# Kernel tuning notes

Measured on AMD Instinct MI355X. Metric: run time of the kernel, lower is better.

The kernel has to match this reference:

```python
import jax, jax.numpy as jnp
import numpy as np

B, S, F_, D, H, L, OUT = 2, 1024, 240, 512, 6, 6, 512
NH = 16
DH = D // NH
EPS = 1e-6  # fast_transformers causal-linear eps
LN_EPS = 1e-5  # torch LayerNorm default


def layernorm(x, g, b):
    m = x.mean(-1, keepdims=True)
    v = ((x - m) ** 2).mean(-1, keepdims=True)
    return (x - m) * jax.lax.rsqrt(v + LN_EPS) * g + b


def causal_linear_attn(q, k, v):
    # q,k,v: [B,S,NH,DH]; feature map phi(x)=elu(x)+1 (fast_transformers default)
    Q = jax.nn.elu(q) + 1.0
    K = jax.nn.elu(k) + 1.0
    # running sum of outer products K_i V_i^T -> [B,S,NH,DH,DH]
    kv = jnp.cumsum(jnp.einsum('bshd,bshm->bshdm', K, v), axis=1)
    num = jnp.einsum('bshd,bshdm->bshm', Q, kv)
    Z = 1.0 / (jnp.einsum('bshd,bshd->bsh', Q, jnp.cumsum(K, axis=1)) + EPS)
    return num * Z[..., None]


def setup_inputs() -> dict:
    key = jax.random.key(0)
    ks = iter(jax.random.split(key, 16))

    def w(shape, s=0.02):
        return (s * jax.random.normal(next(ks), shape)).astype(jnp.float32)

    f32 = jnp.float32
    return {
        'x': jax.random.normal(next(ks), (B, S, F_), dtype=f32),
        'g_in': jnp.ones((F_,), f32), 'b_in': jnp.zeros((F_,), f32),
        'W_pre': w((F_, D)), 'b_pre': jnp.zeros((D,), f32),
        'Wq': w((L, D, D)), 'bq': jnp.zeros((L, D), f32),
        'Wk': w((L, D, D)), 'bk': jnp.zeros((L, D), f32),
        'Wv': w((L, D, D)), 'bv': jnp.zeros((L, D), f32),
        'Wo': w((L, D, D)), 'bo': jnp.zeros((L, D), f32),
        'W1': w((L, D, D)), 'bf1': jnp.zeros((L, D), f32),  # feed_forward_dimensions == hidden_sz
        'W2': w((L, D, D)), 'bf2': jnp.zeros((L, D), f32),
        'ln1_g': jnp.ones((L, D), f32), 'ln1_b': jnp.zeros((L, D), f32),
        'ln2_g': jnp.ones((L, D), f32), 'ln2_b': jnp.zeros((L, D), f32),
        'lnf_g': jnp.ones((D,), f32), 'lnf_b': jnp.zeros((D,), f32),
        'W_post': w((D, OUT)), 'b_post': jnp.zeros((OUT,), f32),
    }


def reference(x, g_in, b_in, W_pre, b_pre, Wq, bq, Wk, bk, Wv, bv, Wo, bo,
              W1, bf1, W2, bf2, ln1_g, ln1_b, ln2_g, ln2_b, lnf_g, lnf_b,
              W_post, b_post):
    # input norm + pre projection
    h = layernorm(x, g_in, b_in) @ W_pre + b_pre  # [B,S,D]
    # fast_transformers post-norm encoder layers
    for l in range(L):
        q = (h @ Wq[l] + bq[l]).reshape(B, S, NH, DH)
        k = (h @ Wk[l] + bk[l]).reshape(B, S, NH, DH)
        v = (h @ Wv[l] + bv[l]).reshape(B, S, NH, DH)
        a = causal_linear_attn(q, k, v).reshape(B, S, D) @ Wo[l] + bo[l]
        h = layernorm(h + a, ln1_g[l], ln1_b[l])
        y = jax.nn.relu(h @ W1[l] + bf1[l]) @ W2[l] + bf2[l]
        h = layernorm(h + y, ln2_g[l], ln2_b[l])
    # final encoder norm, then post projection
    h = layernorm(h, lnf_g, lnf_b)
    return h @ W_post + b_post
```

## Files before the change

### kernel.cpp

```cpp
#include <hip/hip_runtime.h>
#include <hip/hip_bf16.h>
#include <cmath>

#define NROW 2048
#define DMODEL 512
#define FIN 240
#define FINPAD 256
#define NHEAD 16
#define DHEAD 32
#define CHUNK 64
#define NCHUNK 16
#define NLAYER 6
#define SEQ 1024
#define QKVLD 1536

typedef __attribute__((ext_vector_type(8))) short bf16x8;
typedef __attribute__((ext_vector_type(4))) float f32x4;

#define MFMA_BF16 __builtin_amdgcn_mfma_f32_16x16x32_bf16

__device__ __forceinline__ float phi(float x) {
    return x > 0.f ? x + 1.f : expf(x);
}

__device__ __forceinline__ void load_lds16(const void* g, void* l) {
    __builtin_amdgcn_global_load_lds(
        (const __attribute__((address_space(1))) void*)g,
        (__attribute__((address_space(3))) void*)l, 16, 0, 0);
}

__global__ __launch_bounds__(256) void ln_kernel(
    const float* __restrict__ in, const float* __restrict__ res,
    const float* __restrict__ g, const float* __restrict__ b,
    float* __restrict__ out, __hip_bfloat16* __restrict__ outb,
    int C, int Cpad) {
    int row = blockIdx.x;
    int tid = threadIdx.x;
    const float* xr = in + (size_t)row * C;
    const float* rr = res ? res + (size_t)row * C : nullptr;
    float vals[2];
    float sum = 0.f, sq = 0.f;
#pragma unroll
    for (int i = 0; i < 2; ++i) {
        int c = tid + i * 256;
        float v = 0.f;
        if (c < C) { v = xr[c]; if (rr) v += rr[c]; }
        vals[i] = v;
        sum += v; sq += v * v;
    }
#pragma unroll
    for (int off = 32; off > 0; off >>= 1) {
        sum += __shfl_xor(sum, off, 64);
        sq  += __shfl_xor(sq,  off, 64);
    }
    __shared__ float red[8];
    int wv = tid >> 6, ln = tid & 63;
    if (ln == 0) { red[wv] = sum; red[4 + wv] = sq; }
    __syncthreads();
    sum = red[0] + red[1] + red[2] + red[3];
    sq  = red[4] + red[5] + red[6] + red[7];
    float mean = sum / (float)C;
    float var  = sq / (float)C - mean * mean;
    float rstd = rsqrtf(var + 1e-5f);
#pragma unroll
    for (int i = 0; i < 2; ++i) {
        int c = tid + i * 256;
        float y = (vals[i] - mean) * rstd;
        if (c < C) {
            y = y * g[c] + b[c];
            if (out) out[(size_t)row * C + c] = y;
        }
        if (outb && c < Cpad)
            outb[(size_t)row * Cpad + c] = __float2bfloat16(c < C ? y : 0.f);
    }
}

template<int RELU, int WF32, int WBF16, int PHI, int K>
__global__ __launch_bounds__(256) void gemm_bf16_kernel(
    const __hip_bfloat16* __restrict__ A, const __hip_bfloat16* __restrict__ Bt,
    const float* __restrict__ bias,
    float* __restrict__ C, __hip_bfloat16* __restrict__ Cb,
    int N) {
    constexpr int NSTEP = K / 64;
    __shared__ __align__(16) __hip_bfloat16 As[4][32][64];
    __shared__ __align__(16) __hip_bfloat16 Bs[4][64][64];
    const int tid = threadIdx.x, lane = tid & 63, w = tid >> 6;
    const int nN = N >> 6;
    const int bm = (blockIdx.x / nN) * 32;
    const int bn = (blockIdx.x % nN) * 64;

    const int srow  = lane >> 3;
    const int sslot = (lane & 7) ^ srow;
    const size_t aoff = (size_t)srow * K + (size_t)sslot * 8;
    const __hip_bfloat16* gA  = A  + (size_t)(bm + w * 8) * K + aoff;
    const __hip_bfloat16* gB0 = Bt + (size_t)(bn + w * 8) * K + aoff;
    const __hip_bfloat16* gB1 = Bt + (size_t)(bn + 32 + w * 8) * K + aoff;

#define STAGE(t) do { \
        load_lds16(gA  + (size_t)(t) * 64, &As[(t) & 3][w * 8][0]); \
        load_lds16(gB0 + (size_t)(t) * 64, &Bs[(t) & 3][w * 8][0]); \
        load_lds16(gB1 + (size_t)(t) * 64, &Bs[(t) & 3][32 + w * 8][0]); \
    } while (0)

    const int wm = (w >> 1) << 4, wn = (w & 1) << 5;
    const int fr = lane & 15, fq = lane >> 4;
    const int sw = fr & 7;
    const int e0 = ((fq      ^ sw) << 3);
    const int e1 = (((fq | 4) ^ sw) << 3);
    f32x4 acc0 = {0.f, 0.f, 0.f, 0.f}, acc1 = acc0;

    STAGE(0); STAGE(1); STAGE(2);
#pragma unroll
    for (int t = 0; t < NSTEP; ++t) {
        if (NSTEP - t >= 3)      asm volatile("s_waitcnt vmcnt(6)" ::: "memory");
        else if (NSTEP - t == 2) asm volatile("s_waitcnt vmcnt(3)" ::: "memory");
        else                     asm volatile("s_waitcnt vmcnt(0)" ::: "memory");
        __builtin_amdgcn_s_barrier();
        __builtin_amdgcn_sched_barrier(0);
        if (t + 3 < NSTEP) STAGE(t + 3);
        const int b = t & 3;
        bf16x8 a0  = *(const bf16x8*)&As[b][wm + fr][e0];
        bf16x8 a1  = *(const bf16x8*)&As[b][wm + fr][e1];
        bf16x8 b00 = *(const bf16x8*)&Bs[b][wn + fr][e0];
        bf16x8 b01 = *(const bf16x8*)&Bs[b][wn + fr][e1];
        bf16x8 b10 = *(const bf16x8*)&Bs[b][wn + 16 + fr][e0];
        bf16x8 b11 = *(const bf16x8*)&Bs[b][wn + 16 + fr][e1];
        acc0 = MFMA_BF16(a0, b00, acc0, 0, 0, 0);
        acc1 = MFMA_BF16(a0, b10, acc1, 0, 0, 0);
        acc0 = MFMA_BF16(a1, b01, acc0, 0, 0, 0);
        acc1 = MFMA_BF16(a1, b11, acc1, 0, 0, 0);
    }
#undef STAGE

    const int orow = bm + wm + (fq << 2);
    const int ocol = bn + wn + fr;
    float bv0 = bias[ocol], bv1 = bias[ocol + 16];
#pragma unroll
    for (int r = 0; r < 4; ++r) {
        float v0 = acc0[r] + bv0;
        float v1 = acc1[r] + bv1;
        if (RELU) { v0 = fmaxf(v0, 0.f); v1 = fmaxf(v1, 0.f); }
        if (PHI) {
            if (ocol < 1024)      v0 = phi(v0);
            if (ocol + 16 < 1024) v1 = phi(v1);
        }
        if (WF32) {
            C[(size_t)(orow + r) * N + ocol]      = v0;
            C[(size_t)(orow + r) * N + ocol + 16] = v1;
        }
        if (WBF16) {
            Cb[(size_t)(orow + r) * N + ocol]      = __float2bfloat16(v0);
            Cb[(size_t)(orow + r) * N + ocol + 16] = __float2bfloat16(v1);
        }
    }
}

__global__ __launch_bounds__(256) void wconv_kernel(
    const float* __restrict__ W_pre, const float* __restrict__ Wq,
    const float* __restrict__ Wk, const float* __restrict__ Wv,
    const float* __restrict__ Wo, const float* __restrict__ W1,
    const float* __restrict__ W2, const float* __restrict__ W_post,
    const float* __restrict__ bq, const float* __restrict__ bk,
    const float* __restrict__ bv, float* __restrict__ qkvbias,
    __hip_bfloat16* wpre_t, __hip_bfloat16* wqkv_t, __hip_bfloat16* wo_t,
    __hip_bfloat16* w1_t, __hip_bfloat16* w2_t, __hip_bfloat16* wpost_t) {
    __shared__ float tile[64][65];
    int tb = blockIdx.x;
    if (tb >= 2400) {
        int l = tb - 2400;
        for (int i = threadIdx.x; i < 512; i += 256) {
            qkvbias[l * QKVLD + i]        = bq[l * DMODEL + i];
            qkvbias[l * QKVLD + 512 + i]  = bk[l * DMODEL + i];
            qkvbias[l * QKVLD + 1024 + i] = bv[l * DMODEL + i];
        }
        return;
    }
    const float* src; __hip_bfloat16* dst; int K, Kpad, kt, nt;
    if (tb < 32) {
        src = W_pre; dst = wpre_t; K = FIN; Kpad = FINPAD;
        kt = tb >> 3; nt = tb & 7;
    } else {
        int t2 = tb - 32; int mat = t2 >> 6; int tt = t2 & 63;
        kt = tt >> 3; nt = tt & 7; K = 512; Kpad = 512;
        if (mat == 36) { src = W_post; dst = wpost_t; }
        else {
            int l = mat / 6, j = mat % 6;
            const size_t WSZ = 262144;
            switch (j) {
                case 0: src = Wq + l * WSZ; dst = wqkv_t + l * 786432;          break;
                case 1: src = Wk + l * WSZ; dst = wqkv_t + l * 786432 + 262144; break;
                case 2: src = Wv + l * WSZ; dst = wqkv_t + l * 786432 + 524288; break;
                case 3: src = Wo + l * WSZ; dst = wo_t + l * WSZ;               break;
                case 4: src = W1 + l * WSZ; dst = w1_t + l * WSZ;               break;
                default: src = W2 + l * WSZ; dst = w2_t + l * WSZ;              break;
            }
        }
    }
    const int N = 512;
    int t = threadIdx.x;
    int k0 = kt * 64, n0 = nt * 64;
#pragma unroll
    for (int i = 0; i < 16; ++i) {
        int kk = (t >> 6) * 16 + i;
        int nn = t & 63;
        int k = k0 + kk;
        tile[kk][nn] = (k < K) ? src[(size_t)k * N + n0 + nn] : 0.f;
    }
    __syncthreads();
#pragma unroll
    for (int i = 0; i < 16; ++i) {
        int nn = (t >> 6) * 16 + i;
        int kk = t & 63;
        dst[(size_t)(n0 + nn) * Kpad + k0 + kk] = __float2bfloat16(tile[kk][nn]);
    }
}

__global__ __launch_bounds__(64) void attn_state_kernel(
    const __hip_bfloat16* __restrict__ qkvb,
    float* __restrict__ Sg, float* __restrict__ ksumg) {
    __shared__ __hip_bfloat16 Kt[32][72];
    __shared__ __hip_bfloat16 Vt[32][72];
    int c = blockIdx.x, hh = blockIdx.y, b = blockIdx.z;
    int t = threadIdx.x;
    int sub = t >> 2, slot = t & 3;
    size_t rb = ((size_t)(b * SEQ + c * CHUNK)) * QKVLD + hh * DHEAD;
#pragma unroll
    for (int it = 0; it < 4; ++it) {
        int s = it * 16 + sub;
        bf16x8 kv = *(const bf16x8*)&qkvb[rb + (size_t)s * QKVLD + 512 + slot * 8];
        bf16x8 vv = *(const bf16x8*)&qkvb[rb + (size_t)s * QKVLD + 1024 + slot * 8];
#pragma unroll
        for (int i = 0; i < 8; ++i) {
            Kt[slot * 8 + i][s] = ((const __hip_bfloat16*)&kv)[i];
            Vt[slot * 8 + i][s] = ((const __hip_bfloat16*)&vv)[i];
        }
    }
    __syncthreads();
    int fr = t & 15, fq = t >> 4;
    f32x4 a00 = {0.f,0.f,0.f,0.f}, a01 = a00, a10 = a00, a11 = a00;
#pragma unroll
    for (int ks = 0; ks < 2; ++ks) {
        bf16x8 v0 = *(const bf16x8*)&Vt[fr][ks * 32 + fq * 8];
        bf16x8 v1 = *(const bf16x8*)&Vt[16 + fr][ks * 32 + fq * 8];
        bf16x8 k0 = *(const bf16x8*)&Kt[fr][ks * 32 + fq * 8];
        bf16x8 k1 = *(const bf16x8*)&Kt[16 + fr][ks * 32 + fq * 8];
        a00 = MFMA_BF16(v0, k0, a00, 0, 0, 0);
        a01 = MFMA_BF16(v0, k1, a01, 0, 0, 0);
        a10 = MFMA_BF16(v1, k0, a10, 0, 0, 0);
        a11 = MFMA_BF16(v1, k1, a11, 0, 0, 0);
    }
    size_t ob = ((size_t)((b * NHEAD + hh) * NCHUNK + c)) * 1024;
#pragma unroll
    for (int r = 0; r < 4; ++r) {
        int m0 = fq * 4 + r;
        Sg[ob + (size_t)m0 * 32 + fr]             = a00[r];
        Sg[ob + (size_t)m0 * 32 + 16 + fr]        = a01[r];
        Sg[ob + (size_t)(16 + m0) * 32 + fr]      = a10[r];
        Sg[ob + (size_t)(16 + m0) * 32 + 16 + fr] = a11[r];
    }
    if (t < 32) {
        float s_ = 0.f;
        for (int s = 0; s < CHUNK; ++s) s_ += __bfloat162float(Kt[t][s]);
        ksumg[((size_t)((b * NHEAD + hh) * NCHUNK + c)) * 32 + t] = s_;
    }
}

__global__ __launch_bounds__(256) void attn_out_kernel(
    const __hip_bfloat16* __restrict__ qkvb,
    const float* __restrict__ Sg, const float* __restrict__ ksumg,
    __hip_bfloat16* __restrict__ out) {
    __shared__ __hip_bfloat16 Qs[64][40];
    __shared__ __hip_bfloat16 Ks[64][40];
    __shared__ __hip_bfloat16 Vt[32][72];
    __shared__ __hip_bfloat16 Awb[64][72];
    __shared__ __hip_bfloat16 Stb[32][40];
    __shared__ float den[64];
    __shared__ float ksml[32];
    int c = blockIdx.x, hh = blockIdx.y, b = blockIdx.z;
    int tid = threadIdx.x, lane = tid & 63, w = tid >> 6;
    size_t rb = ((size_t)(b * SEQ + c * CHUNK)) * QKVLD + hh * DHEAD;
    {
        int row = tid >> 2, slot = tid & 3;
        *(bf16x8*)&Qs[row][slot * 8] =
            *(const bf16x8*)&qkvb[rb + (size_t)row * QKVLD + slot * 8];
        *(bf16x8*)&Ks[row][slot * 8] =
            *(const bf16x8*)&qkvb[rb + (size_t)row * QKVLD + 512 + slot * 8];
        bf16x8 vv = *(const bf16x8*)&qkvb[rb + (size_t)row * QKVLD + 1024 + slot * 8];
        if (row < 64) {
#pragma unroll
            for (int i = 0; i < 8; ++i)
                Vt[slot * 8 + i][row] = ((const __hip_bfloat16*)&vv)[i];
        }
    }
    size_t sb = ((size_t)((b * NHEAD + hh) * NCHUNK)) * 1024;
    {
        f32x4 st = {0.f, 0.f, 0.f, 0.f};
        for (int cp = 0; cp < c; ++cp)
            st += *(const f32x4*)&Sg[sb + (size_t)cp * 1024 + tid * 4];
        int m = tid >> 3, d0 = (tid & 7) * 4;
#pragma unroll
        for (int i = 0; i < 4; ++i) Stb[m][d0 + i] = __float2bfloat16(st[i]);
    }
    if (tid < 32) {
        size_t kb = ((size_t)((b * NHEAD + hh) * NCHUNK)) * 32;
        float s_ = 0.f;
        for (int cp = 0; cp < c; ++cp) s_ += ksumg[kb + cp * 32 + tid];
        ksml[tid] = s_;
    }
    __syncthreads();
    int fr = lane & 15, fq = lane >> 4;
    bf16x8 aQ = *(const bf16x8*)&Qs[w * 16 + fr][fq * 8];
    f32x4 p[4];
#pragma unroll
    for (int j = 0; j < 4; ++j) {
        f32x4 z = {0.f, 0.f, 0.f, 0.f};
        bf16x8 bK = *(const bf16x8*)&Ks[j * 16 + fr][fq * 8];
        p[j] = MFMA_BF16(aQ, bK, z, 0, 0, 0);
    }
    float rs[4] = {0.f, 0.f, 0.f, 0.f};
#pragma unroll
    for (int j = 0; j < 4; ++j) {
        int tcol = j * 16 + fr;
#pragma unroll
        for (int r = 0; r < 4; ++r) {
            int s = w * 16 + fq * 4 + r;
            float val = (tcol <= s) ? p[j][r] : 0.f;
            p[j][r] = val;
            rs[r] += val;
        }
    }
#pragma unroll
    for (int off = 8; off > 0; off >>= 1) {
#pragma unroll
        for (int r = 0; r < 4; ++r) rs[r] += __shfl_xor(rs[r], off, 64);
    }
    if (fr == 0) {
#pragma unroll
        for (int r = 0; r < 4; ++r) den[w * 16 + fq * 4 + r] = rs[r];
    }
#pragma unroll
    for (int j = 0; j < 4; ++j)
#pragma unroll
        for (int r = 0; r < 4; ++r)
            Awb[w * 16 + fq * 4 + r][j * 16 + fr] = __float2bfloat16(p[j][r]);
    __syncthreads();
    if (tid < 64) {
        float dq = den[tid];
        float dst_ = 0.f;
#pragma unroll
        for (int d = 0; d < 32; ++d)
            dst_ += __bfloat162float(Qs[tid][d]) * ksml[d];
        den[tid] = 1.f / (dq + dst_ + 1e-6f);
    }
    __syncthreads();
    size_t orb = ((size_t)(b * SEQ + c * CHUNK)) * DMODEL + hh * DHEAD;
#pragma unroll
    for (int mf = 0; mf < 2; ++mf) {
        f32x4 acc = {0.f, 0.f, 0.f, 0.f};
        bf16x8 bS = *(const bf16x8*)&Stb[mf * 16 + fr][fq * 8];
        acc = MFMA_BF16(aQ, bS, acc, 0, 0, 0);
#pragma unroll
        for (int ks = 0; ks < 2; ++ks) {
            bf16x8 aA = *(const bf16x8*)&Awb[w * 16 + fr][ks * 32 + fq * 8];
            bf16x8 bV = *(const bf16x8*)&Vt[mf * 16 + fr][ks * 32 + fq * 8];
            acc = MFMA_BF16(aA, bV, acc, 0, 0, 0);
        }
#pragma unroll
        for (int r = 0; r < 4; ++r) {
            int s = w * 16 + fq * 4 + r;
            out[orb + (size_t)s * DMODEL + mf * 16 + fr] =
                __float2bfloat16(acc[r] * den[s]);
        }
    }
}

template<int R, int WF, int WB, int PHI, int K>
static inline void gemm(const __hip_bfloat16* A, const __hip_bfloat16* Bt,
                        const float* bias, float* C, __hip_bfloat16* Cb,
                        int M, int N, hipStream_t s) {
    gemm_bf16_kernel<R, WF, WB, PHI, K><<<(M / 32) * (N / 64), 256, 0, s>>>(A, Bt, bias, C, Cb, N);
}

extern "C" void kernel_launch(void* const* d_in, const int* in_sizes, int n_in,
                              void* d_out, int out_size, void* d_ws, size_t ws_size,
                              hipStream_t stream) {
    const float* x      = (const float*)d_in[0];
    const float* g_in   = (const float*)d_in[1];
    const float* b_in   = (const float*)d_in[2];
    const float* W_pre  = (const float*)d_in[3];
    const float* b_pre  = (const float*)d_in[4];
    const float* Wq     = (const float*)d_in[5];
    const float* bq     = (const float*)d_in[6];
    const float* Wk     = (const float*)d_in[7];
    const float* bk     = (const float*)d_in[8];
    const float* Wv     = (const float*)d_in[9];
    const float* bv     = (const float*)d_in[10];
    const float* Wo     = (const float*)d_in[11];
    const float* bo     = (const float*)d_in[12];
    const float* W1     = (const float*)d_in[13];
    const float* bf1    = (const float*)d_in[14];
    const float* W2     = (const float*)d_in[15];
    const float* bf2    = (const float*)d_in[16];
    const float* ln1_g  = (const float*)d_in[17];
    const float* ln1_b  = (const float*)d_in[18];
    const float* ln2_g  = (const float*)d_in[19];
    const float* ln2_b  = (const float*)d_in[20];
    const float* lnf_g  = (const float*)d_in[21];
    const float* lnf_b  = (const float*)d_in[22];
    const float* W_post = (const float*)d_in[23];
    const float* b_post = (const float*)d_in[24];
    (void)in_sizes; (void)n_in; (void)out_size; (void)ws_size;

    float* ws = (float*)d_ws;
    const size_t SZ = (size_t)NROW * DMODEL;
    float* h       = ws;
    float* t1      = h + SZ;
    float* Sg      = t1 + SZ;
    float* ksumg   = Sg + 524288;
    float* qkvbias = ksumg + 16384;
    __hip_bfloat16* bp = (__hip_bfloat16*)(qkvbias + 9216);
    __hip_bfloat16* hb     = bp;            bp += SZ;
    __hip_bfloat16* qkvb   = bp;            bp += (size_t)NROW * QKVLD;
    __hip_bfloat16* xnb    = bp;            bp += (size_t)NROW * FINPAD;
    __hip_bfloat16* attb   = bp;            bp += SZ;
    __hip_bfloat16* ffb    = bp;            bp += SZ;
    __hip_bfloat16* t0b    = bp;            bp += SZ;
    __hip_bfloat16* wpre_t = bp;            bp += (size_t)DMODEL * FINPAD;
    __hip_bfloat16* wqkv_t = bp;            bp += (size_t)NLAYER * 786432;
    __hip_bfloat16* wo_t   = bp;            bp += (size_t)NLAYER * 262144;
    __hip_bfloat16* w1_t   = bp;            bp += (size_t)NLAYER * 262144;
    __hip_bfloat16* w2_t   = bp;            bp += (size_t)NLAYER * 262144;
    __hip_bfloat16* wpost_t= bp;

    wconv_kernel<<<2406, 256, 0, stream>>>(
        W_pre, Wq, Wk, Wv, Wo, W1, W2, W_post,
        bq, bk, bv, qkvbias,
        wpre_t, wqkv_t, wo_t, w1_t, w2_t, wpost_t);

    ln_kernel<<<NROW, 256, 0, stream>>>(x, nullptr, g_in, b_in, nullptr, xnb, FIN, FINPAD);
    gemm<0, 1, 1, 0, FINPAD>(xnb, wpre_t, b_pre, h, hb, NROW, DMODEL, stream);

    dim3 ag(NCHUNK, NHEAD, 2);
    for (int l = 0; l < NLAYER; ++l) {
        gemm<0, 0, 1, 1, DMODEL>(hb, wqkv_t + (size_t)l * 786432, qkvbias + l * QKVLD,
                                 nullptr, qkvb, NROW, QKVLD, stream);
        attn_state_kernel<<<ag, 64, 0, stream>>>(qkvb, Sg, ksumg);
        attn_out_kernel<<<ag, 256, 0, stream>>>(qkvb, Sg, ksumg, attb);
        gemm<0, 1, 0, 0, DMODEL>(attb, wo_t + (size_t)l * 262144, bo + l * DMODEL,
                                 t1, nullptr, NROW, DMODEL, stream);
        ln_kernel<<<NROW, 256, 0, stream>>>(h, t1, ln1_g + l * DMODEL, ln1_b + l * DMODEL,
                                            h, hb, DMODEL, DMODEL);
        gemm<1, 0, 1, 0, DMODEL>(hb, w1_t + (size_t)l * 262144, bf1 + l * DMODEL,
                                 nullptr, ffb, NROW, DMODEL, stream);
        gemm<0, 1, 0, 0, DMODEL>(ffb, w2_t + (size_t)l * 262144, bf2 + l * DMODEL,
                                 t1, nullptr, NROW, DMODEL, stream);
        ln_kernel<<<NROW, 256, 0, stream>>>(h, t1, ln2_g + l * DMODEL, ln2_b + l * DMODEL,
                                            h, hb, DMODEL, DMODEL);
    }

    ln_kernel<<<NROW, 256, 0, stream>>>(h, nullptr, lnf_g, lnf_b, nullptr, t0b, DMODEL, DMODEL);
    gemm<0, 1, 0, 0, DMODEL>(t0b, wpost_t, b_post, (float*)d_out, nullptr, NROW, DMODEL, stream);
}
```

Measured before the change: 368.0 us.

## Enlarge GEMM tile to 64x64, vectorize single-wave layernorm, store chunk states in bf16

The GEMM block tile grows from 32x64 to 64x64, so each wave computes four MFMA accumulators and reuses the loaded A and B fragments more, at the cost of half as many blocks. LayerNorm moves to a single 64-thread wave with float4 loads and stores, which removes the LDS reduction and barrier. Per-chunk attention KV states are written and read as bf16 instead of fp32, cutting memory traffic in exchange for some precision. The attn_out V-transpose also drops a redundant row guard.

```diff
diff --git a/kernel.cpp b/kernel.cpp
--- a/kernel.cpp
+++ b/kernel.cpp
@@ -16,11 +16,21 @@
 
 typedef __attribute__((ext_vector_type(8))) short bf16x8;
 typedef __attribute__((ext_vector_type(4))) float f32x4;
+typedef __attribute__((ext_vector_type(4))) unsigned short u16x4;
 
 #define MFMA_BF16 __builtin_amdgcn_mfma_f32_16x16x32_bf16
 
 __device__ __forceinline__ float phi(float x) {
     return x > 0.f ? x + 1.f : expf(x);
+}
+
+__device__ __forceinline__ float bf2f(unsigned short u) {
+    return __uint_as_float((unsigned)u << 16);
+}
+
+__device__ __forceinline__ unsigned short f2bf_bits(float z) {
+    __hip_bfloat16 hb_ = __float2bfloat16(z);
+    return *reinterpret_cast<unsigned short*>(&hb_);
 }
 
 __device__ __forceinline__ void load_lds16(const void* g, void* l) {
@@ -29,49 +39,58 @@
         (__attribute__((address_space(3))) void*)l, 16, 0, 0);
 }
 
-__global__ __launch_bounds__(256) void ln_kernel(
+__global__ __launch_bounds__(64) void ln_kernel(
     const float* __restrict__ in, const float* __restrict__ res,
     const float* __restrict__ g, const float* __restrict__ b,
     float* __restrict__ out, __hip_bfloat16* __restrict__ outb,
     int C, int Cpad) {
     int row = blockIdx.x;
-    int tid = threadIdx.x;
+    int t = threadIdx.x;
     const float* xr = in + (size_t)row * C;
     const float* rr = res ? res + (size_t)row * C : nullptr;
-    float vals[2];
+    f32x4 v[2] = {{0.f,0.f,0.f,0.f},{0.f,0.f,0.f,0.f}};
     float sum = 0.f, sq = 0.f;
 #pragma unroll
     for (int i = 0; i < 2; ++i) {
-        int c = tid + i * 256;
-        float v = 0.f;
-        if (c < C) { v = xr[c]; if (rr) v += rr[c]; }
-        vals[i] = v;
-        sum += v; sq += v * v;
+        int c = (t + i * 64) * 4;
+        if (c < C) {
+            f32x4 x_ = *(const f32x4*)&xr[c];
+            if (rr) x_ += *(const f32x4*)&rr[c];
+            v[i] = x_;
+#pragma unroll
+            for (int j = 0; j < 4; ++j) { sum += x_[j]; sq += x_[j] * x_[j]; }
+        }
     }
 #pragma unroll
     for (int off = 32; off > 0; off >>= 1) {
         sum += __shfl_xor(sum, off, 64);
         sq  += __shfl_xor(sq,  off, 64);
     }
-    __shared__ float red[8];
-    int wv = tid >> 6, ln = tid & 63;
-    if (ln == 0) { red[wv] = sum; red[4 + wv] = sq; }
-    __syncthreads();
-    sum = red[0] + red[1] + red[2] + red[3];
-    sq  = red[4] + red[5] + red[6] + red[7];
     float mean = sum / (float)C;
     float var  = sq / (float)C - mean * mean;
     float rstd = rsqrtf(var + 1e-5f);
 #pragma unroll
     for (int i = 0; i < 2; ++i) {
-        int c = tid + i * 256;
-        float y = (vals[i] - mean) * rstd;
+        int c = (t + i * 64) * 4;
+        f32x4 y;
+#pragma unroll
+        for (int j = 0; j < 4; ++j) y[j] = (v[i][j] - mean) * rstd;
         if (c < C) {
-            y = y * g[c] + b[c];
-            if (out) out[(size_t)row * C + c] = y;
-        }
-        if (outb && c < Cpad)
-            outb[(size_t)row * Cpad + c] = __float2bfloat16(c < C ? y : 0.f);
+            f32x4 gg = *(const f32x4*)&g[c];
+            f32x4 bb = *(const f32x4*)&b[c];
+#pragma unroll
+            for (int j = 0; j < 4; ++j) y[j] = y[j] * gg[j] + bb[j];
+            if (out) *(f32x4*)&out[(size_t)row * C + c] = y;
+        }
+        if (outb && c < Cpad) {
+            u16x4 o;
+#pragma unroll
+            for (int j = 0; j < 4; ++j) {
+                float z = (c + j < C) ? y[j] : 0.f;
+                o[j] = f2bf_bits(z);
+            }
+            *(u16x4*)&outb[(size_t)row * Cpad + c] = o;
+        }
     }
 }
 
@@ -82,77 +101,89 @@
     float* __restrict__ C, __hip_bfloat16* __restrict__ Cb,
     int N) {
     constexpr int NSTEP = K / 64;
-    __shared__ __align__(16) __hip_bfloat16 As[4][32][64];
+    __shared__ __align__(16) __hip_bfloat16 As[4][64][64];
     __shared__ __align__(16) __hip_bfloat16 Bs[4][64][64];
     const int tid = threadIdx.x, lane = tid & 63, w = tid >> 6;
     const int nN = N >> 6;
-    const int bm = (blockIdx.x / nN) * 32;
+    const int bm = (blockIdx.x / nN) * 64;
     const int bn = (blockIdx.x % nN) * 64;
 
     const int srow  = lane >> 3;
     const int sslot = (lane & 7) ^ srow;
     const size_t aoff = (size_t)srow * K + (size_t)sslot * 8;
-    const __hip_bfloat16* gA  = A  + (size_t)(bm + w * 8) * K + aoff;
+    const __hip_bfloat16* gA0 = A  + (size_t)(bm + w * 8) * K + aoff;
+    const __hip_bfloat16* gA1 = A  + (size_t)(bm + 32 + w * 8) * K + aoff;
     const __hip_bfloat16* gB0 = Bt + (size_t)(bn + w * 8) * K + aoff;
     const __hip_bfloat16* gB1 = Bt + (size_t)(bn + 32 + w * 8) * K + aoff;
 
 #define STAGE(t) do { \
-        load_lds16(gA  + (size_t)(t) * 64, &As[(t) & 3][w * 8][0]); \
+        load_lds16(gA0 + (size_t)(t) * 64, &As[(t) & 3][w * 8][0]); \
+        load_lds16(gA1 + (size_t)(t) * 64, &As[(t) & 3][32 + w * 8][0]); \
         load_lds16(gB0 + (size_t)(t) * 64, &Bs[(t) & 3][w * 8][0]); \
         load_lds16(gB1 + (size_t)(t) * 64, &Bs[(t) & 3][32 + w * 8][0]); \
     } while (0)
 
-    const int wm = (w >> 1) << 4, wn = (w & 1) << 5;
+    const int wm = (w >> 1) << 5, wn = (w & 1) << 5;
     const int fr = lane & 15, fq = lane >> 4;
     const int sw = fr & 7;
     const int e0 = ((fq      ^ sw) << 3);
     const int e1 = (((fq | 4) ^ sw) << 3);
-    f32x4 acc0 = {0.f, 0.f, 0.f, 0.f}, acc1 = acc0;
+    f32x4 acc00 = {0.f, 0.f, 0.f, 0.f}, acc01 = acc00, acc10 = acc00, acc11 = acc00;
 
     STAGE(0); STAGE(1); STAGE(2);
 #pragma unroll
     for (int t = 0; t < NSTEP; ++t) {
-        if (NSTEP - t >= 3)      asm volatile("s_waitcnt vmcnt(6)" ::: "memory");
-        else if (NSTEP - t == 2) asm volatile("s_waitcnt vmcnt(3)" ::: "memory");
+        if (NSTEP - t >= 3)      asm volatile("s_waitcnt vmcnt(8)" ::: "memory");
+        else if (NSTEP - t == 2) asm volatile("s_waitcnt vmcnt(4)" ::: "memory");
         else                     asm volatile("s_waitcnt vmcnt(0)" ::: "memory");
         __builtin_amdgcn_s_barrier();
         __builtin_amdgcn_sched_barrier(0);
         if (t + 3 < NSTEP) STAGE(t + 3);
         const int b = t & 3;
-        bf16x8 a0  = *(const bf16x8*)&As[b][wm + fr][e0];
-        bf16x8 a1  = *(const bf16x8*)&As[b][wm + fr][e1];
+        bf16x8 a00 = *(const bf16x8*)&As[b][wm + fr][e0];
+        bf16x8 a01 = *(const bf16x8*)&As[b][wm + fr][e1];
+        bf16x8 a10 = *(const bf16x8*)&As[b][wm + 16 + fr][e0];
+        bf16x8 a11 = *(const bf16x8*)&As[b][wm + 16 + fr][e1];
         bf16x8 b00 = *(const bf16x8*)&Bs[b][wn + fr][e0];
         bf16x8 b01 = *(const bf16x8*)&Bs[b][wn + fr][e1];
         bf16x8 b10 = *(const bf16x8*)&Bs[b][wn + 16 + fr][e0];
         bf16x8 b11 = *(const bf16x8*)&Bs[b][wn + 16 + fr][e1];
-        acc0 = MFMA_BF16(a0, b00, acc0, 0, 0, 0);
-        acc1 = MFMA_BF16(a0, b10, acc1, 0, 0, 0);
-        acc0 = MFMA_BF16(a1, b01, acc0, 0, 0, 0);
-        acc1 = MFMA_BF16(a1, b11, acc1, 0, 0, 0);
+        acc00 = MFMA_BF16(a00, b00, acc00, 0, 0, 0);
+        acc01 = MFMA_BF16(a00, b10, acc01, 0, 0, 0);
+        acc10 = MFMA_BF16(a10, b00, acc10, 0, 0, 0);
+        acc11 = MFMA_BF16(a10, b10, acc11, 0, 0, 0);
+        acc00 = MFMA_BF16(a01, b01, acc00, 0, 0, 0);
+        acc01 = MFMA_BF16(a01, b11, acc01, 0, 0, 0);
+        acc10 = MFMA_BF16(a11, b01, acc10, 0, 0, 0);
+        acc11 = MFMA_BF16(a11, b11, acc11, 0, 0, 0);
     }
 #undef STAGE
 
     const int orow = bm + wm + (fq << 2);
     const int ocol = bn + wn + fr;
     float bv0 = bias[ocol], bv1 = bias[ocol + 16];
-#pragma unroll
-    for (int r = 0; r < 4; ++r) {
-        float v0 = acc0[r] + bv0;
-        float v1 = acc1[r] + bv1;
-        if (RELU) { v0 = fmaxf(v0, 0.f); v1 = fmaxf(v1, 0.f); }
-        if (PHI) {
-            if (ocol < 1024)      v0 = phi(v0);
-            if (ocol + 16 < 1024) v1 = phi(v1);
-        }
-        if (WF32) {
-            C[(size_t)(orow + r) * N + ocol]      = v0;
-            C[(size_t)(orow + r) * N + ocol + 16] = v1;
-        }
-        if (WBF16) {
-            Cb[(size_t)(orow + r) * N + ocol]      = __float2bfloat16(v0);
-            Cb[(size_t)(orow + r) * N + ocol + 16] = __float2bfloat16(v1);
-        }
-    }
+    f32x4 accs[2][2] = {{acc00, acc01}, {acc10, acc11}};
+#pragma unroll
+    for (int i = 0; i < 2; ++i)
+#pragma unroll
+        for (int r = 0; r < 4; ++r) {
+            int row = orow + i * 16 + r;
+            float v0 = accs[i][0][r] + bv0;
+            float v1 = accs[i][1][r] + bv1;
+            if (RELU) { v0 = fmaxf(v0, 0.f); v1 = fmaxf(v1, 0.f); }
+            if (PHI) {
+                if (ocol < 1024)      v0 = phi(v0);
+                if (ocol + 16 < 1024) v1 = phi(v1);
+            }
+            if (WF32) {
+                C[(size_t)row * N + ocol]      = v0;
+                C[(size_t)row * N + ocol + 16] = v1;
+            }
+            if (WBF16) {
+                Cb[(size_t)row * N + ocol]      = __float2bfloat16(v0);
+                Cb[(size_t)row * N + ocol + 16] = __float2bfloat16(v1);
+            }
+        }
 }
 
 __global__ __launch_bounds__(256) void wconv_kernel(
@@ -217,7 +248,7 @@
 
 __global__ __launch_bounds__(64) void attn_state_kernel(
     const __hip_bfloat16* __restrict__ qkvb,
-    float* __restrict__ Sg, float* __restrict__ ksumg) {
+    __hip_bfloat16* __restrict__ Sg, float* __restrict__ ksumg) {
     __shared__ __hip_bfloat16 Kt[32][72];
     __shared__ __hip_bfloat16 Vt[32][72];
     int c = blockIdx.x, hh = blockIdx.y, b = blockIdx.z;
@@ -253,10 +284,10 @@
 #pragma unroll
     for (int r = 0; r < 4; ++r) {
         int m0 = fq * 4 + r;
-        Sg[ob + (size_t)m0 * 32 + fr]             = a00[r];
-        Sg[ob + (size_t)m0 * 32 + 16 + fr]        = a01[r];
-        Sg[ob + (size_t)(16 + m0) * 32 + fr]      = a10[r];
-        Sg[ob + (size_t)(16 + m0) * 32 + 16 + fr] = a11[r];
+        Sg[ob + (size_t)m0 * 32 + fr]             = __float2bfloat16(a00[r]);
+        Sg[ob + (size_t)m0 * 32 + 16 + fr]        = __float2bfloat16(a01[r]);
+        Sg[ob + (size_t)(16 + m0) * 32 + fr]      = __float2bfloat16(a10[r]);
+        Sg[ob + (size_t)(16 + m0) * 32 + 16 + fr] = __float2bfloat16(a11[r]);
     }
     if (t < 32) {
         float s_ = 0.f;
@@ -267,7 +298,7 @@
 
 __global__ __launch_bounds__(256) void attn_out_kernel(
     const __hip_bfloat16* __restrict__ qkvb,
-    const float* __restrict__ Sg, const float* __restrict__ ksumg,
+    const __hip_bfloat16* __restrict__ Sg, const float* __restrict__ ksumg,
     __hip_bfloat16* __restrict__ out) {
     __shared__ __hip_bfloat16 Qs[64][40];
     __shared__ __hip_bfloat16 Ks[64][40];
@@ -286,17 +317,18 @@
         *(bf16x8*)&Ks[row][slot * 8] =
             *(const bf16x8*)&qkvb[rb + (size_t)row * QKVLD + 512 + slot * 8];
         bf16x8 vv = *(const bf16x8*)&qkvb[rb + (size_t)row * QKVLD + 1024 + slot * 8];
-        if (row < 64) {
-#pragma unroll
-            for (int i = 0; i < 8; ++i)
-                Vt[slot * 8 + i][row] = ((const __hip_bfloat16*)&vv)[i];
-        }
+#pragma unroll
+        for (int i = 0; i < 8; ++i)
+            Vt[slot * 8 + i][row] = ((const __hip_bfloat16*)&vv)[i];
     }
     size_t sb = ((size_t)((b * NHEAD + hh) * NCHUNK)) * 1024;
     {
         f32x4 st = {0.f, 0.f, 0.f, 0.f};
-        for (int cp = 0; cp < c; ++cp)
-            st += *(const f32x4*)&Sg[sb + (size_t)cp * 1024 + tid * 4];
+        for (int cp = 0; cp < c; ++cp) {
+            u16x4 sv = *(const u16x4*)&Sg[sb + (size_t)cp * 1024 + tid * 4];
+#pragma unroll
+            for (int i = 0; i < 4; ++i) st[i] += bf2f(sv[i]);
+        }
         int m = tid >> 3, d0 = (tid & 7) * 4;
 #pragma unroll
         for (int i = 0; i < 4; ++i) Stb[m][d0 + i] = __float2bfloat16(st[i]);
@@ -378,7 +410,7 @@
 static inline void gemm(const __hip_bfloat16* A, const __hip_bfloat16* Bt,
                         const float* bias, float* C, __hip_bfloat16* Cb,
                         int M, int N, hipStream_t s) {
-    gemm_bf16_kernel<R, WF, WB, PHI, K><<<(M / 32) * (N / 64), 256, 0, s>>>(A, Bt, bias, C, Cb, N);
+    gemm_bf16_kernel<R, WF, WB, PHI, K><<<(M / 64) * (N / 64), 256, 0, s>>>(A, Bt, bias, C, Cb, N);
 }
 
 extern "C" void kernel_launch(void* const* d_in, const int* in_sizes, int n_in,
@@ -415,10 +447,10 @@
     const size_t SZ = (size_t)NROW * DMODEL;
     float* h       = ws;
     float* t1      = h + SZ;
-    float* Sg      = t1 + SZ;
-    float* ksumg   = Sg + 524288;
+    float* ksumg   = t1 + SZ;
     float* qkvbias = ksumg + 16384;
     __hip_bfloat16* bp = (__hip_bfloat16*)(qkvbias + 9216);
+    __hip_bfloat16* Sg     = bp;            bp += 524288;
     __hip_bfloat16* hb     = bp;            bp += SZ;
     __hip_bfloat16* qkvb   = bp;            bp += (size_t)NROW * QKVLD;
     __hip_bfloat16* xnb    = bp;            bp += (size_t)NROW * FINPAD;
@@ -437,7 +469,7 @@
         bq, bk, bv, qkvbias,
         wpre_t, wqkv_t, wo_t, w1_t, w2_t, wpost_t);
 
-    ln_kernel<<<NROW, 256, 0, stream>>>(x, nullptr, g_in, b_in, nullptr, xnb, FIN, FINPAD);
+    ln_kernel<<<NROW, 64, 0, stream>>>(x, nullptr, g_in, b_in, nullptr, xnb, FIN, FINPAD);
     gemm<0, 1, 1, 0, FINPAD>(xnb, wpre_t, b_pre, h, hb, NROW, DMODEL, stream);
 
     dim3 ag(NCHUNK, NHEAD, 2);
@@ -448,16 +480,16 @@
         attn_out_kernel<<<ag, 256, 0, stream>>>(qkvb, Sg, ksumg, attb);
         gemm<0, 1, 0, 0, DMODEL>(attb, wo_t + (size_t)l * 262144, bo + l * DMODEL,
                                  t1, nullptr, NROW, DMODEL, stream);
-        ln_kernel<<<NROW, 256, 0, stream>>>(h, t1, ln1_g + l * DMODEL, ln1_b + l * DMODEL,
-                                            h, hb, DMODEL, DMODEL);
+        ln_kernel<<<NROW, 64, 0, stream>>>(h, t1, ln1_g + l * DMODEL, ln1_b + l * DMODEL,
+                                           h, hb, DMODEL, DMODEL);
         gemm<1, 0, 1, 0, DMODEL>(hb, w1_t + (size_t)l * 262144, bf1 + l * DMODEL,
                                  nullptr, ffb, NROW, DMODEL, stream);
         gemm<0, 1, 0, 0, DMODEL>(ffb, w2_t + (size_t)l * 262144, bf2 + l * DMODEL,
                                  t1, nullptr, NROW, DMODEL, stream);
-        ln_kernel<<<NROW, 256, 0, stream>>>(h, t1, ln2_g + l * DMODEL, ln2_b + l * DMODEL,
-                                            h, hb, DMODEL, DMODEL);
-    }
-
-    ln_kernel<<<NROW, 256, 0, stream>>>(h, nullptr, lnf_g, lnf_b, nullptr, t0b, DMODEL, DMODEL);
+        ln_kernel<<<NROW, 64, 0, stream>>>(h, t1, ln2_g + l * DMODEL, ln2_b + l * DMODEL,
+                                           h, hb, DMODEL, DMODEL);
+    }
+
+    ln_kernel<<<NROW, 64, 0, stream>>>(h, nullptr, lnf_g, lnf_b, nullptr, t0b, DMODEL, DMODEL);
     gemm<0, 1, 0, 0, DMODEL>(t0b, wpost_t, b_post, (float*)d_out, nullptr, NROW, DMODEL, stream);
 }
```

Result: faster. 346.7 us, median of 2 (-5.8%).
